# Kernel optimization log

Hardware: AMD Instinct MI355X
Metric: run time of the kernel (lower is better)

The kernel has to match this reference:

```python
import jax, jax.numpy as jnp
import numpy as np

N_NODES = 50000
N_EDGES = 800000
N_GRAPHS = 512
IN_CH, H, OUT = 58, 64, 128
HEADS1 = 4
NEG_SLOPE = 0.2
BN_EPS = 1e-5


def setup_inputs() -> dict:
    key = jax.random.key(0)
    ks = jax.random.split(key, 16)
    x = jax.random.normal(ks[0], (N_NODES, IN_CH), dtype=jnp.float32)
    edge_index = jax.random.randint(ks[1], (2, N_EDGES), 0, N_NODES, dtype=jnp.int64)
    batch = jnp.sort(jax.random.randint(ks[2], (N_NODES,), 0, N_GRAPHS, dtype=jnp.int64))
    s = 0.1
    return {
        "x": x,
        "edge_index": edge_index,
        "batch": batch,
        "W1": jax.random.normal(ks[3], (IN_CH, HEADS1 * H), dtype=jnp.float32) * s,
        "att_src1": jax.random.normal(ks[4], (HEADS1, H), dtype=jnp.float32) * s,
        "att_dst1": jax.random.normal(ks[5], (HEADS1, H), dtype=jnp.float32) * s,
        "b1": jnp.zeros((HEADS1 * H,), dtype=jnp.float32),
        "W2": jax.random.normal(ks[6], (HEADS1 * H, OUT), dtype=jnp.float32) * s,
        "att_src2": jax.random.normal(ks[7], (1, OUT), dtype=jnp.float32) * s,
        "att_dst2": jax.random.normal(ks[8], (1, OUT), dtype=jnp.float32) * s,
        "b2": jnp.zeros((OUT,), dtype=jnp.float32),
        "gamma": jax.random.normal(ks[9], (OUT,), dtype=jnp.float32) * 0.1 + 1.0,
        "beta": jax.random.normal(ks[10], (OUT,), dtype=jnp.float32) * 0.1,
    }


def gat_conv(x, src, dst, W, att_src, att_dst, b, heads, d_out):
    """PyG GATConv (concat=True, dropout off), self-loops already in src/dst."""
    n = x.shape[0]
    h = (x @ W).reshape(n, heads, d_out)                 # [N,H,D]
    a_s = jnp.einsum("nhd,hd->nh", h, att_src)            # [N,H]
    a_d = jnp.einsum("nhd,hd->nh", h, att_dst)            # [N,H]
    e = jax.nn.leaky_relu(a_s[src] + a_d[dst], NEG_SLOPE)  # [E,H]
    # softmax over edges grouped by destination node
    m = jax.ops.segment_max(e, dst, num_segments=n)
    ex = jnp.exp(e - m[dst])
    z = jax.ops.segment_sum(ex, dst, num_segments=n)
    alpha = ex / (z[dst] + 1e-16)
    msg = h[src] * alpha[:, :, None]                      # [E,H,D]
    out = jax.ops.segment_sum(msg, dst, num_segments=n)   # [N,H,D]
    return out.reshape(n, heads * d_out) + b


def reference(x, edge_index, batch, W1, att_src1, att_dst1, b1,
              W2, att_src2, att_dst2, b2, gamma, beta):
    n = x.shape[0]
    loops = jnp.arange(n, dtype=edge_index.dtype)
    src = jnp.concatenate([edge_index[0], loops])
    dst = jnp.concatenate([edge_index[1], loops])

    h1 = jax.nn.relu(gat_conv(x, src, dst, W1, att_src1, att_dst1, b1, HEADS1, H))
    h2 = jax.nn.relu(gat_conv(h1, src, dst, W2, att_src2, att_dst2, b2, 1, OUT))

    # global mean pool over graphs
    sums = jax.ops.segment_sum(h2, batch, num_segments=N_GRAPHS)      # [G,OUT]
    cnt = jax.ops.segment_sum(jnp.ones((n,), h2.dtype), batch, num_segments=N_GRAPHS)
    pooled = sums / jnp.maximum(cnt, 1.0)[:, None]

    # BatchNorm1d, training mode (batch statistics, biased variance)
    mu = pooled.mean(axis=0)
    var = pooled.var(axis=0)
    return (pooled - mu) / jnp.sqrt(var + BN_EPS) * gamma + beta
```

## Files before the change

kernel.cpp:

```cpp
#include <hip/hip_runtime.h>
#include <hip/hip_bf16.h>
#include <math.h>

#define N_NODES  50000
#define N_EDGES  800000
#define E_TOT    850000
#define N_GRAPHS 512
#define IN_CH    58
#define K1P      64
#define C1       256
#define H1       4
#define C2       128
#define NEG_SLOPE 0.2f
#define SLOT_CAP 64
#define NBUILD   208
#define NATT     3125
#define NBUCK    196
#define BCAP     5120

typedef __attribute__((ext_vector_type(8))) short short8;
typedef __attribute__((ext_vector_type(4))) float f32x4;

__device__ __forceinline__ float lo16(unsigned u) { return __uint_as_float(u << 16); }
__device__ __forceinline__ float hi16(unsigned u) { return __uint_as_float(u & 0xffff0000u); }
__device__ __forceinline__ float leaky(float e) { return e > 0.f ? e : NEG_SLOPE * e; }
__device__ __forceinline__ unsigned short f2bfu(float v) {
    __hip_bfloat16 b = __float2bfloat16(v);
    return *(unsigned short*)&b;
}
__device__ __forceinline__ unsigned pack2(float lo, float hi) {
    return (unsigned)f2bfu(lo) | ((unsigned)f2bfu(hi) << 16);
}

__global__ __launch_bounds__(256) void k_frontA(const float* __restrict__ W1,
                                                const float* __restrict__ W2,
                                                const float* __restrict__ atts1,
                                                const float* __restrict__ attd1,
                                                unsigned short* __restrict__ w1p,
                                                unsigned short* __restrict__ w2p,
                                                float* __restrict__ wproj) {
    int b = blockIdx.x;
    int t = threadIdx.x;
    if (b < 256) {
        if (t < K1P) {
            float v = (t < IN_CH) ? W1[t * C1 + b] : 0.f;
            int h = b >> 6, jj = (b >> 4) & 3, l15 = b & 15;
            int kk = t >> 5, quad = (t >> 3) & 3, e = t & 7;
            int f = (h * 4 + jj) * 2 + kk;
            w1p[(f * 64 + l15 * 4 + quad) * 8 + e] = f2bfu(v);
        }
    } else if (b < 384) {
        int n = b - 256;
        int j = n >> 4, l15 = n & 15;
        int k0 = t >> 5, quad = (t >> 3) & 3, e = t & 7;
        int f = j * 8 + k0;
        w2p[(f * 64 + l15 * 4 + quad) * 8 + e] = f2bfu(W2[t * C2 + n]);
    } else {
        int k = t >> 2, h = t & 3;
        float s = 0.f, dd = 0.f;
        if (k < IN_CH) {
            for (int j = 0; j < 64; ++j) {
                float wv = W1[k * C1 + h * 64 + j];
                s  += wv * atts1[h * 64 + j];
                dd += wv * attd1[h * 64 + j];
            }
        }
        wproj[t] = s;
        wproj[256 + t] = dd;
    }
}

__global__ __launch_bounds__(256) void k_mid(const int* __restrict__ src,
                                             const int* __restrict__ dst,
                                             int* __restrict__ bcnt,
                                             uint2* __restrict__ ebuf,
                                             const float* __restrict__ x,
                                             const float* __restrict__ wproj,
                                             unsigned short* __restrict__ xbf,
                                             float* __restrict__ a_s,
                                             float* __restrict__ a_d) {
    __shared__ int lhist[NBUCK];
    __shared__ int lbase[NBUCK];
    int b = blockIdx.x;
    int t = threadIdx.x;
    if (b < NBUILD) {
        if (t < NBUCK) lhist[t] = 0;
        __syncthreads();
        int j0 = (b * 256 + t) * 16;
        int s[16], d[16], bk[16], lp[16];
        bool v[16];
#pragma unroll
        for (int k = 0; k < 16; ++k) {
            int j = j0 + k;
            v[k] = j < E_TOT;
            if (v[k]) {
                if (j < N_EDGES) { s[k] = src[j]; d[k] = dst[j]; }
                else             { s[k] = d[k] = j - N_EDGES; }
                bk[k] = d[k] >> 8;
            }
        }
#pragma unroll
        for (int k = 0; k < 16; ++k)
            if (v[k]) lp[k] = atomicAdd(&lhist[bk[k]], 1);
        __syncthreads();
        if (t < NBUCK) lbase[t] = atomicAdd(&bcnt[t], lhist[t]);
        __syncthreads();
#pragma unroll
        for (int k = 0; k < 16; ++k)
            if (v[k])
                ebuf[(size_t)bk[k] * BCAP + lbase[bk[k]] + lp[k]] =
                    make_uint2((unsigned)s[k], (unsigned)d[k]);
    } else {
        int wave = t >> 6, lane = t & 63;
        int q = lane >> 4, hl = lane & 15;
        int n = (b - NBUILD) * 16 + wave * 4 + q;
        float xa[4] = {0.f, 0.f, 0.f, 0.f};
        const float* xr = x + (size_t)n * IN_CH + hl * 4;
        if (hl < 14) {
            float4 xv = *(const float4*)xr;
            xa[0] = xv.x; xa[1] = xv.y; xa[2] = xv.z; xa[3] = xv.w;
        } else if (hl == 14) {
            xa[0] = xr[0]; xa[1] = xr[1];
        }
        ((uint2*)xbf)[n * 16 + hl] = make_uint2(pack2(xa[0], xa[1]), pack2(xa[2], xa[3]));
        float ps[4] = {0.f, 0.f, 0.f, 0.f}, pd[4] = {0.f, 0.f, 0.f, 0.f};
#pragma unroll
        for (int cc = 0; cc < 4; ++cc) {
            int c = hl * 4 + cc;
            float4 wsv = *(const float4*)(wproj + c * 4);
            float4 wdv = *(const float4*)(wproj + 256 + c * 4);
            ps[0] += xa[cc] * wsv.x; ps[1] += xa[cc] * wsv.y;
            ps[2] += xa[cc] * wsv.z; ps[3] += xa[cc] * wsv.w;
            pd[0] += xa[cc] * wdv.x; pd[1] += xa[cc] * wdv.y;
            pd[2] += xa[cc] * wdv.z; pd[3] += xa[cc] * wdv.w;
        }
#pragma unroll
        for (int o = 8; o > 0; o >>= 1) {
#pragma unroll
            for (int r = 0; r < 4; ++r) {
                ps[r] += __shfl_down(ps[r], o, 16);
                pd[r] += __shfl_down(pd[r], o, 16);
            }
        }
        if (hl == 0) {
            *(float4*)(a_s + n * 4) = make_float4(ps[0], ps[1], ps[2], ps[3]);
            *(float4*)(a_d + n * 4) = make_float4(pd[0], pd[1], pd[2], pd[3]);
        }
    }
}

__global__ __launch_bounds__(256) void k_scat(const int* __restrict__ bcnt,
                                              const uint2* __restrict__ ebuf,
                                              int* __restrict__ deg,
                                              int* __restrict__ slots) {
    __shared__ int ldeg[256];
    int blk = blockIdx.x, t = threadIdx.x;
    ldeg[t] = 0;
    __syncthreads();
    int cnt = bcnt[blk];
    const uint2* eb = ebuf + (size_t)blk * BCAP;
    int base = 0;
    for (; base + 1024 <= cnt; base += 1024) {
        uint2 e[4];
#pragma unroll
        for (int k = 0; k < 4; ++k) e[k] = eb[base + k * 256 + t];
#pragma unroll
        for (int k = 0; k < 4; ++k) {
            int pos = atomicAdd(&ldeg[e[k].y & 255], 1);
            slots[((int)e[k].y << 6) + pos] = (int)e[k].x;
        }
    }
    for (int i = base + t; i < cnt; i += 256) {
        uint2 e = eb[i];
        int pos = atomicAdd(&ldeg[e.y & 255], 1);
        slots[((int)e.y << 6) + pos] = (int)e.x;
    }
    __syncthreads();
    int g = (blk << 8) + t;
    if (g < N_NODES) deg[g] = ldeg[t];
}

__global__ __launch_bounds__(256) void k_l1_agg(const int* __restrict__ degv,
                                                const int* __restrict__ slots,
                                                const float* __restrict__ a_s,
                                                const float* __restrict__ a_d,
                                                const uint2* __restrict__ xbf,
                                                unsigned short* __restrict__ xagg) {
    int t = threadIdx.x;
    int wave = t >> 6, lane = t & 63;
    int q = lane >> 4, hl = lane & 15;
    int d = blockIdx.x * 16 + wave * 4 + q;
    int beg = d << 6;
    int deg = degv[d];
    float4 ad = *(const float4*)(a_d + d * 4);
    float z0 = 0.f, z1 = 0.f, z2 = 0.f, z3 = 0.f;
    float a0[4] = {0.f, 0.f, 0.f, 0.f};
    float a1[4] = {0.f, 0.f, 0.f, 0.f};
    float a2[4] = {0.f, 0.f, 0.f, 0.f};
    float a3[4] = {0.f, 0.f, 0.f, 0.f};
    int i = 0;
    for (; i + 8 <= deg; i += 8) {
        int e0 = beg + i;
        int s[8]; uint2 u[8]; float4 as[8];
#pragma unroll
        for (int k = 0; k < 8; ++k) s[k] = slots[e0 + k];
#pragma unroll
        for (int k = 0; k < 8; ++k) u[k] = xbf[s[k] * 16 + hl];
#pragma unroll
        for (int k = 0; k < 8; ++k) as[k] = *(const float4*)(a_s + s[k] * 4);
#pragma unroll
        for (int k = 0; k < 8; ++k) {
            float e0h = __expf(leaky(as[k].x + ad.x));
            float e1h = __expf(leaky(as[k].y + ad.y));
            float e2h = __expf(leaky(as[k].z + ad.z));
            float e3h = __expf(leaky(as[k].w + ad.w));
            z0 += e0h; z1 += e1h; z2 += e2h; z3 += e3h;
            float c0 = lo16(u[k].x), c1 = hi16(u[k].x);
            float c2 = lo16(u[k].y), c3 = hi16(u[k].y);
            a0[0] += e0h * c0; a0[1] += e0h * c1; a0[2] += e0h * c2; a0[3] += e0h * c3;
            a1[0] += e1h * c0; a1[1] += e1h * c1; a1[2] += e1h * c2; a1[3] += e1h * c3;
            a2[0] += e2h * c0; a2[1] += e2h * c1; a2[2] += e2h * c2; a2[3] += e2h * c3;
            a3[0] += e3h * c0; a3[1] += e3h * c1; a3[2] += e3h * c2; a3[3] += e3h * c3;
        }
    }
    for (; i < deg; ++i) {
        int s = slots[beg + i];
        uint2 u = xbf[s * 16 + hl];
        float4 as = *(const float4*)(a_s + s * 4);
        float e0h = __expf(leaky(as.x + ad.x));
        float e1h = __expf(leaky(as.y + ad.y));
        float e2h = __expf(leaky(as.z + ad.z));
        float e3h = __expf(leaky(as.w + ad.w));
        z0 += e0h; z1 += e1h; z2 += e2h; z3 += e3h;
        float c0 = lo16(u.x), c1 = hi16(u.x);
        float c2 = lo16(u.y), c3 = hi16(u.y);
        a0[0] += e0h * c0; a0[1] += e0h * c1; a0[2] += e0h * c2; a0[3] += e0h * c3;
        a1[0] += e1h * c0; a1[1] += e1h * c1; a1[2] += e1h * c2; a1[3] += e1h * c3;
        a2[0] += e2h * c0; a2[1] += e2h * c1; a2[2] += e2h * c2; a2[3] += e2h * c3;
        a3[0] += e3h * c0; a3[1] += e3h * c1; a3[2] += e3h * c2; a3[3] += e3h * c3;
    }
    float i0 = 1.f / z0, i1 = 1.f / z1, i2 = 1.f / z2, i3 = 1.f / z3;
    int T = d >> 4, r = d & 15;
    int kk = hl >> 3, qd = (hl >> 1) & 3, half = hl & 1;
    uint2* xo = (uint2*)xagg;
    int base = (((T * 8 + kk) * 64) + r * 4 + qd) * 2 + half;
    xo[base +   0] = make_uint2(pack2(a0[0] * i0, a0[1] * i0), pack2(a0[2] * i0, a0[3] * i0));
    xo[base + 256] = make_uint2(pack2(a1[0] * i1, a1[1] * i1), pack2(a1[2] * i1, a1[3] * i1));
    xo[base + 512] = make_uint2(pack2(a2[0] * i2, a2[1] * i2), pack2(a2[2] * i2, a2[3] * i2));
    xo[base + 768] = make_uint2(pack2(a3[0] * i3, a3[1] * i3), pack2(a3[2] * i3, a3[3] * i3));
}

__global__ __launch_bounds__(256) void k_gemm12(const unsigned short* __restrict__ xagg,
                                                const unsigned short* __restrict__ w1p,
                                                const float* __restrict__ b1v,
                                                const unsigned short* __restrict__ w2p,
                                                const float* __restrict__ atts,
                                                const float* __restrict__ attd,
                                                unsigned short* __restrict__ h2bf,
                                                float* __restrict__ a_s,
                                                float* __restrict__ a_d) {
    __shared__ unsigned short hlds[4][16][264];
    int t = threadIdx.x;
    int wave = t >> 6, lane = t & 63;
    int T = blockIdx.x * 4 + wave;
    int m0 = T * 16;
    int l15 = lane & 15, quad = lane >> 4;
    int fl = l15 * 4 + quad;
    bool active = m0 < N_NODES;

    if (active) {
        const short8* xf  = (const short8*)xagg + (size_t)T * 512 + fl;
        const short8* w1f = (const short8*)w1p + fl;
        short8 av[H1][2];
#pragma unroll
        for (int h = 0; h < H1; ++h) {
            av[h][0] = xf[(h * 2 + 0) * 64];
            av[h][1] = xf[(h * 2 + 1) * 64];
        }
#pragma unroll
        for (int h = 0; h < H1; ++h) {
            short8 wb0[4], wb1[4];
#pragma unroll
            for (int jj = 0; jj < 4; ++jj) {
                wb0[jj] = w1f[(((h * 4 + jj) * 2) + 0) * 64];
                wb1[jj] = w1f[(((h * 4 + jj) * 2) + 1) * 64];
            }
            f32x4 acc[4];
#pragma unroll
            for (int jj = 0; jj < 4; ++jj) {
                acc[jj] = (f32x4){0.f, 0.f, 0.f, 0.f};
                acc[jj] = __builtin_amdgcn_mfma_f32_16x16x32_bf16(av[h][0], wb0[jj], acc[jj], 0, 0, 0);
                acc[jj] = __builtin_amdgcn_mfma_f32_16x16x32_bf16(av[h][1], wb1[jj], acc[jj], 0, 0, 0);
            }
#pragma unroll
            for (int jj = 0; jj < 4; ++jj) {
                int c = h * 64 + jj * 16 + l15;
                float bb = b1v[c];
#pragma unroll
                for (int r = 0; r < 4; ++r)
                    hlds[wave][quad * 4 + r][c] = f2bfu(fmaxf(acc[jj][r] + bb, 0.f));
            }
        }
    }
    __syncthreads();
    if (!active) return;

    short8 a2[8];
    const unsigned short* a2row = &hlds[wave][l15][0] + quad * 8;
#pragma unroll
    for (int k0 = 0; k0 < 8; ++k0) a2[k0] = *(const short8*)(a2row + k0 * 32);

    const short8* w2f = (const short8*)w2p + fl;
    unsigned short* scr = &hlds[wave][0][0];
    float ps[4] = {0.f, 0.f, 0.f, 0.f}, pd[4] = {0.f, 0.f, 0.f, 0.f};
#pragma unroll
    for (int j = 0; j < 8; ++j) {
        short8 wb[8];
#pragma unroll
        for (int k0 = 0; k0 < 8; ++k0)
            wb[k0] = w2f[(j * 8 + k0) * 64];
        f32x4 acc = (f32x4){0.f, 0.f, 0.f, 0.f};
#pragma unroll
        for (int k0 = 0; k0 < 8; ++k0)
            acc = __builtin_amdgcn_mfma_f32_16x16x32_bf16(a2[k0], wb[k0], acc, 0, 0, 0);
        float as_ = atts[j * 16 + l15], ad_ = attd[j * 16 + l15];
#pragma unroll
        for (int r = 0; r < 4; ++r) {
            float v = acc[r];
            scr[(quad * 4 + r) * 136 + j * 16 + l15] = f2bfu(v);
            ps[r] += v * as_;
            pd[r] += v * ad_;
        }
    }
#pragma unroll
    for (int r = 0; r < 4; ++r) {
#pragma unroll
        for (int o = 8; o > 0; o >>= 1) {
            ps[r] += __shfl_down(ps[r], o, 16);
            pd[r] += __shfl_down(pd[r], o, 16);
        }
        if (l15 == 0) {
            int n = m0 + quad * 4 + r;
            a_s[n] = ps[r];
            a_d[n] = pd[r];
        }
    }
    int row = lane >> 2, seg = lane & 3;
#pragma unroll
    for (int c = 0; c < 4; ++c) {
        short8 v = *(const short8*)(scr + row * 136 + (c * 4 + seg) * 8);
        *(short8*)(h2bf + (size_t)(m0 + row) * C2 + (c * 4 + seg) * 8) = v;
    }
}

__global__ __launch_bounds__(256) void k_l2_aggpool(const int* __restrict__ degv,
                                                    const int* __restrict__ slots,
                                                    const float* __restrict__ a_s,
                                                    const float* __restrict__ a_d,
                                                    const unsigned short* __restrict__ h2bf,
                                                    const float* __restrict__ b2,
                                                    const int* __restrict__ batch,
                                                    float* __restrict__ pooled) {
    __shared__ float sacc[8][C2];
    __shared__ int sg[8];
    int t = threadIdx.x;
    int wave = t >> 6, lane = t & 63;
    int half = lane >> 5, hl = lane & 31;
    int nodeIdx = wave * 2 + half;
    int d = blockIdx.x * 8 + nodeIdx;
    int beg = d << 6;
    int deg = degv[d];
    float ad = a_d[d];
    const uint2* rows = (const uint2*)h2bf;
    float a0 = 0.f, a1 = 0.f, a2 = 0.f, a3 = 0.f, z = 0.f;
    int i = 0;
    for (; i + 8 <= deg; i += 8) {
        int e0 = beg + i;
        int s[8]; uint2 u[8]; float ex[8];
#pragma unroll
        for (int k = 0; k < 8; ++k) s[k] = slots[e0 + k];
#pragma unroll
        for (int k = 0; k < 8; ++k) u[k] = rows[s[k] * 32 + hl];
#pragma unroll
        for (int k = 0; k < 8; ++k) ex[k] = __expf(leaky(a_s[s[k]] + ad));
#pragma unroll
        for (int k = 0; k < 8; ++k) {
            z  += ex[k];
            a0 += ex[k] * lo16(u[k].x); a1 += ex[k] * hi16(u[k].x);
            a2 += ex[k] * lo16(u[k].y); a3 += ex[k] * hi16(u[k].y);
        }
    }
    for (; i < deg; ++i) {
        int s = slots[beg + i];
        uint2 u = rows[s * 32 + hl];
        float ex = __expf(leaky(a_s[s] + ad));
        z  += ex;
        a0 += ex * lo16(u.x); a1 += ex * hi16(u.x);
        a2 += ex * lo16(u.y); a3 += ex * hi16(u.y);
    }
    float inv = 1.f / z;
    int c = hl * 4;
    float4 bv = *(const float4*)(b2 + c);
    float v0 = fmaxf(a0 * inv + bv.x, 0.f);
    float v1 = fmaxf(a1 * inv + bv.y, 0.f);
    float v2 = fmaxf(a2 * inv + bv.z, 0.f);
    float v3 = fmaxf(a3 * inv + bv.w, 0.f);
    if (hl == 0) sg[nodeIdx] = batch[d];
    *(float4*)&sacc[nodeIdx][c] = make_float4(v0, v1, v2, v3);
    __syncthreads();
    if (t < C2) {
        float run = sacc[0][t];
        int gprev = sg[0];
#pragma unroll
        for (int j = 1; j < 8; ++j) {
            int gj = sg[j];
            float v = sacc[j][t];
            if (gj == gprev) {
                run += v;
            } else {
                atomicAdd(&pooled[gprev * C2 + t], run);
                run = v;
                gprev = gj;
            }
        }
        atomicAdd(&pooled[gprev * C2 + t], run);
    }
}

__global__ __launch_bounds__(512) void k_bn(const float* __restrict__ pooled,
                                            const int* __restrict__ batch,
                                            const float* __restrict__ gamma,
                                            const float* __restrict__ beta,
                                            float* __restrict__ out) {
    int c = blockIdx.x;
    int g = threadIdx.x;
    int lo = 0, hi = N_NODES;
    while (lo < hi) { int m = (lo + hi) >> 1; if (batch[m] < g) lo = m + 1; else hi = m; }
    int lo2 = lo, hi2 = N_NODES;
    while (lo2 < hi2) { int m = (lo2 + hi2) >> 1; if (batch[m] < g + 1) lo2 = m + 1; else hi2 = m; }
    float cntg = (float)(hi2 - lo);

    __shared__ float red[512];
    __shared__ float s_mu, s_var;
    float v = pooled[g * C2 + c] / fmaxf(cntg, 1.0f);
    red[g] = v;
    __syncthreads();
    for (int s = 256; s > 0; s >>= 1) {
        if (g < s) red[g] += red[g + s];
        __syncthreads();
    }
    if (g == 0) s_mu = red[0] * (1.0f / N_GRAPHS);
    __syncthreads();
    float dv = v - s_mu;
    red[g] = dv * dv;
    __syncthreads();
    for (int s = 256; s > 0; s >>= 1) {
        if (g < s) red[g] += red[g + s];
        __syncthreads();
    }
    if (g == 0) s_var = red[0] * (1.0f / N_GRAPHS);
    __syncthreads();
    out[g * C2 + c] = dv * rsqrtf(s_var + 1e-5f) * gamma[c] + beta[c];
}

extern "C" void kernel_launch(void* const* d_in, const int* in_sizes, int n_in,
                              void* d_out, int out_size, void* d_ws, size_t ws_size,
                              hipStream_t stream) {
    const float* x     = (const float*)d_in[0];
    const int*   eidx  = (const int*)d_in[1];
    const int*   batch = (const int*)d_in[2];
    const float* W1    = (const float*)d_in[3];
    const float* atts1 = (const float*)d_in[4];
    const float* attd1 = (const float*)d_in[5];
    const float* b1    = (const float*)d_in[6];
    const float* W2    = (const float*)d_in[7];
    const float* atts2 = (const float*)d_in[8];
    const float* attd2 = (const float*)d_in[9];
    const float* b2    = (const float*)d_in[10];
    const float* gamma = (const float*)d_in[11];
    const float* beta  = (const float*)d_in[12];
    float* out = (float*)d_out;
    float* ws  = (float*)d_ws;

    const int* src = eidx;
    const int* dst = eidx + N_EDGES;

    const size_t o_xbf    = 0;
    const size_t o_xagg   = 1600000;
    const size_t o_h2bf   = 8000000;
    const size_t o_w1p    = 11200000;
    const size_t o_w2p    = 11208192;
    const size_t o_wproj  = 11224576;
    const size_t o_as1    = 11225088;
    const size_t o_ad1    = 11425088;
    const size_t o_as2    = 11625088;
    const size_t o_ad2    = 11675088;
    const size_t o_slots  = 11725088;
    const size_t o_deg    = 14925088;
    const size_t o_pool   = 14975088;
    const size_t o_bcnt   = 15040624;
    const size_t total    = 15040880;

    int* p_slots = (int*)(ws + o_slots);
    int* p_deg   = (int*)(ws + o_deg);
    int* p_bcnt  = (int*)(ws + o_bcnt);
    uint2* p_ebuf = (uint2*)(ws + o_xagg);
    unsigned short* p_xbf  = (unsigned short*)(ws + o_xbf);
    unsigned short* p_xagg = (unsigned short*)(ws + o_xagg);
    unsigned short* p_h2bf = (unsigned short*)(ws + o_h2bf);
    unsigned short* p_w1p  = (unsigned short*)(ws + o_w1p);
    unsigned short* p_w2p  = (unsigned short*)(ws + o_w2p);

    hipMemsetAsync(ws + o_deg, 0, (total - o_deg) * sizeof(float), stream);

    k_frontA<<<385, 256, 0, stream>>>(W1, W2, atts1, attd1,
                                      p_w1p, p_w2p, ws + o_wproj);
    k_mid<<<NBUILD + NATT, 256, 0, stream>>>(src, dst, p_bcnt, p_ebuf,
                                             x, ws + o_wproj, p_xbf,
                                             ws + o_as1, ws + o_ad1);
    k_scat<<<NBUCK, 256, 0, stream>>>(p_bcnt, p_ebuf, p_deg, p_slots);

    const int nagg1 = N_NODES / 16;
    const int nagg2 = N_NODES / 8;
    const int nmfma = (N_NODES + 63) / 64;

    k_l1_agg<<<nagg1, 256, 0, stream>>>(p_deg, p_slots, ws + o_as1, ws + o_ad1,
                                        (const uint2*)p_xbf, p_xagg);
    k_gemm12<<<nmfma, 256, 0, stream>>>(p_xagg, p_w1p, b1, p_w2p, atts2, attd2,
                                        p_h2bf, ws + o_as2, ws + o_ad2);

    k_l2_aggpool<<<nagg2, 256, 0, stream>>>(p_deg, p_slots, ws + o_as2, ws + o_ad2,
                                            p_h2bf, b2, batch, ws + o_pool);

    k_bn<<<C2, 512, 0, stream>>>(ws + o_pool, batch, gamma, beta, out);
}
```

Before: 244.5 us.

## Precompute normalized attention weights once per edge before GAT aggregations

In layer 1, each wave now computes the softmax-normalized edge weights for its four destination nodes once, lane-parallel over the slot list, and stores them as bf16 in LDS. The gather loop then reads these weights instead of recomputing exp per feature lane. For layer 2, a new kernel packs the bf16-normalized weight into the upper 16 bits of each slot entry, so the aggregation reads index and weight with one load and uses wider uint4 row loads, covering 16 nodes per block. The normalization drops the max-subtraction and rounds weights to bf16, which loses precision, and the 16-bit source index depends on N_NODES fitting in 65536.

```diff
diff --git a/kernel.cpp b/kernel.cpp
--- a/kernel.cpp
+++ b/kernel.cpp
@@ -186,35 +186,58 @@
                                                 const float* __restrict__ a_d,
                                                 const uint2* __restrict__ xbf,
                                                 unsigned short* __restrict__ xagg) {
+    __shared__ uint2 wlds[4][4][SLOT_CAP];
     int t = threadIdx.x;
     int wave = t >> 6, lane = t & 63;
     int q = lane >> 4, hl = lane & 15;
-    int d = blockIdx.x * 16 + wave * 4 + q;
+    int dbase = blockIdx.x * 16 + wave * 4;
+
+#pragma unroll
+    for (int nn = 0; nn < 4; ++nn) {
+        int node = dbase + nn;
+        int dg = degv[node];
+        float w0 = 0.f, w1 = 0.f, w2 = 0.f, w3 = 0.f;
+        if (lane < dg) {
+            int s = slots[(node << 6) + lane];
+            float4 as = *(const float4*)(a_s + s * 4);
+            float4 ad = *(const float4*)(a_d + node * 4);
+            w0 = __expf(leaky(as.x + ad.x));
+            w1 = __expf(leaky(as.y + ad.y));
+            w2 = __expf(leaky(as.z + ad.z));
+            w3 = __expf(leaky(as.w + ad.w));
+        }
+        float z0 = w0, z1 = w1, z2 = w2, z3 = w3;
+#pragma unroll
+        for (int o = 32; o > 0; o >>= 1) {
+            z0 += __shfl_xor(z0, o, 64); z1 += __shfl_xor(z1, o, 64);
+            z2 += __shfl_xor(z2, o, 64); z3 += __shfl_xor(z3, o, 64);
+        }
+        float i0 = 1.f / z0, i1 = 1.f / z1, i2 = 1.f / z2, i3 = 1.f / z3;
+        wlds[wave][nn][lane] = make_uint2(pack2(w0 * i0, w1 * i1), pack2(w2 * i2, w3 * i3));
+    }
+
+    int d = dbase + q;
     int beg = d << 6;
-    int deg = degv[d];
-    float4 ad = *(const float4*)(a_d + d * 4);
-    float z0 = 0.f, z1 = 0.f, z2 = 0.f, z3 = 0.f;
+    int dg = degv[d];
+    const uint2* wrow = &wlds[wave][q][0];
     float a0[4] = {0.f, 0.f, 0.f, 0.f};
     float a1[4] = {0.f, 0.f, 0.f, 0.f};
     float a2[4] = {0.f, 0.f, 0.f, 0.f};
     float a3[4] = {0.f, 0.f, 0.f, 0.f};
     int i = 0;
-    for (; i + 8 <= deg; i += 8) {
+    for (; i + 8 <= dg; i += 8) {
         int e0 = beg + i;
-        int s[8]; uint2 u[8]; float4 as[8];
+        int s[8]; uint2 u[8]; uint2 w[8];
 #pragma unroll
         for (int k = 0; k < 8; ++k) s[k] = slots[e0 + k];
 #pragma unroll
         for (int k = 0; k < 8; ++k) u[k] = xbf[s[k] * 16 + hl];
 #pragma unroll
-        for (int k = 0; k < 8; ++k) as[k] = *(const float4*)(a_s + s[k] * 4);
+        for (int k = 0; k < 8; ++k) w[k] = wrow[i + k];
 #pragma unroll
         for (int k = 0; k < 8; ++k) {
-            float e0h = __expf(leaky(as[k].x + ad.x));
-            float e1h = __expf(leaky(as[k].y + ad.y));
-            float e2h = __expf(leaky(as[k].z + ad.z));
-            float e3h = __expf(leaky(as[k].w + ad.w));
-            z0 += e0h; z1 += e1h; z2 += e2h; z3 += e3h;
+            float e0h = lo16(w[k].x), e1h = hi16(w[k].x);
+            float e2h = lo16(w[k].y), e3h = hi16(w[k].y);
             float c0 = lo16(u[k].x), c1 = hi16(u[k].x);
             float c2 = lo16(u[k].y), c3 = hi16(u[k].y);
             a0[0] += e0h * c0; a0[1] += e0h * c1; a0[2] += e0h * c2; a0[3] += e0h * c3;
@@ -223,15 +246,12 @@
             a3[0] += e3h * c0; a3[1] += e3h * c1; a3[2] += e3h * c2; a3[3] += e3h * c3;
         }
     }
-    for (; i < deg; ++i) {
+    for (; i < dg; ++i) {
         int s = slots[beg + i];
         uint2 u = xbf[s * 16 + hl];
-        float4 as = *(const float4*)(a_s + s * 4);
-        float e0h = __expf(leaky(as.x + ad.x));
-        float e1h = __expf(leaky(as.y + ad.y));
-        float e2h = __expf(leaky(as.z + ad.z));
-        float e3h = __expf(leaky(as.w + ad.w));
-        z0 += e0h; z1 += e1h; z2 += e2h; z3 += e3h;
+        uint2 w = wrow[i];
+        float e0h = lo16(w.x), e1h = hi16(w.x);
+        float e2h = lo16(w.y), e3h = hi16(w.y);
         float c0 = lo16(u.x), c1 = hi16(u.x);
         float c2 = lo16(u.y), c3 = hi16(u.y);
         a0[0] += e0h * c0; a0[1] += e0h * c1; a0[2] += e0h * c2; a0[3] += e0h * c3;
@@ -239,15 +259,14 @@
         a2[0] += e2h * c0; a2[1] += e2h * c1; a2[2] += e2h * c2; a2[3] += e2h * c3;
         a3[0] += e3h * c0; a3[1] += e3h * c1; a3[2] += e3h * c2; a3[3] += e3h * c3;
     }
-    float i0 = 1.f / z0, i1 = 1.f / z1, i2 = 1.f / z2, i3 = 1.f / z3;
     int T = d >> 4, r = d & 15;
     int kk = hl >> 3, qd = (hl >> 1) & 3, half = hl & 1;
     uint2* xo = (uint2*)xagg;
     int base = (((T * 8 + kk) * 64) + r * 4 + qd) * 2 + half;
-    xo[base +   0] = make_uint2(pack2(a0[0] * i0, a0[1] * i0), pack2(a0[2] * i0, a0[3] * i0));
-    xo[base + 256] = make_uint2(pack2(a1[0] * i1, a1[1] * i1), pack2(a1[2] * i1, a1[3] * i1));
-    xo[base + 512] = make_uint2(pack2(a2[0] * i2, a2[1] * i2), pack2(a2[2] * i2, a2[3] * i2));
-    xo[base + 768] = make_uint2(pack2(a3[0] * i3, a3[1] * i3), pack2(a3[2] * i3, a3[3] * i3));
+    xo[base +   0] = make_uint2(pack2(a0[0], a0[1]), pack2(a0[2], a0[3]));
+    xo[base + 256] = make_uint2(pack2(a1[0], a1[1]), pack2(a1[2], a1[3]));
+    xo[base + 512] = make_uint2(pack2(a2[0], a2[1]), pack2(a2[2], a2[3]));
+    xo[base + 768] = make_uint2(pack2(a3[0], a3[1]), pack2(a3[2], a3[3]));
 }
 
 __global__ __launch_bounds__(256) void k_gemm12(const unsigned short* __restrict__ xagg,
@@ -353,66 +372,89 @@
     }
 }
 
+__global__ __launch_bounds__(256) void k_w2(const int* __restrict__ degv,
+                                            int* __restrict__ slots,
+                                            const float* __restrict__ a_s,
+                                            const float* __restrict__ a_d) {
+    int t = threadIdx.x;
+    int wave = t >> 6, lane = t & 63;
+    int node = blockIdx.x * 4 + wave;
+    int dg = degv[node];
+    float ad = a_d[node];
+    float w = 0.f;
+    int s = 0;
+    if (lane < dg) {
+        s = slots[(node << 6) + lane];
+        w = __expf(leaky(a_s[s] + ad));
+    }
+    float z = w;
+#pragma unroll
+    for (int o = 32; o > 0; o >>= 1) z += __shfl_xor(z, o, 64);
+    float wn = w / z;
+    if (lane < dg)
+        slots[(node << 6) + lane] = s | ((unsigned)f2bfu(wn) << 16);
+}
+
 __global__ __launch_bounds__(256) void k_l2_aggpool(const int* __restrict__ degv,
                                                     const int* __restrict__ slots,
-                                                    const float* __restrict__ a_s,
-                                                    const float* __restrict__ a_d,
                                                     const unsigned short* __restrict__ h2bf,
                                                     const float* __restrict__ b2,
                                                     const int* __restrict__ batch,
                                                     float* __restrict__ pooled) {
-    __shared__ float sacc[8][C2];
-    __shared__ int sg[8];
+    __shared__ float sacc[16][C2];
+    __shared__ int sg[16];
     int t = threadIdx.x;
     int wave = t >> 6, lane = t & 63;
-    int half = lane >> 5, hl = lane & 31;
-    int nodeIdx = wave * 2 + half;
-    int d = blockIdx.x * 8 + nodeIdx;
+    int q = lane >> 4, hl = lane & 15;
+    int nodeIdx = wave * 4 + q;
+    int d = blockIdx.x * 16 + nodeIdx;
     int beg = d << 6;
-    int deg = degv[d];
-    float ad = a_d[d];
-    const uint2* rows = (const uint2*)h2bf;
-    float a0 = 0.f, a1 = 0.f, a2 = 0.f, a3 = 0.f, z = 0.f;
+    int dg = degv[d];
+    const uint4* rows = (const uint4*)h2bf;
+    float a0 = 0.f, a1 = 0.f, a2 = 0.f, a3 = 0.f;
+    float a4 = 0.f, a5 = 0.f, a6 = 0.f, a7 = 0.f;
     int i = 0;
-    for (; i + 8 <= deg; i += 8) {
+    for (; i + 8 <= dg; i += 8) {
         int e0 = beg + i;
-        int s[8]; uint2 u[8]; float ex[8];
-#pragma unroll
-        for (int k = 0; k < 8; ++k) s[k] = slots[e0 + k];
-#pragma unroll
-        for (int k = 0; k < 8; ++k) u[k] = rows[s[k] * 32 + hl];
-#pragma unroll
-        for (int k = 0; k < 8; ++k) ex[k] = __expf(leaky(a_s[s[k]] + ad));
+        int e[8]; uint4 u[8];
+#pragma unroll
+        for (int k = 0; k < 8; ++k) e[k] = slots[e0 + k];
+#pragma unroll
+        for (int k = 0; k < 8; ++k) u[k] = rows[(e[k] & 0xFFFF) * 16 + hl];
 #pragma unroll
         for (int k = 0; k < 8; ++k) {
-            z  += ex[k];
-            a0 += ex[k] * lo16(u[k].x); a1 += ex[k] * hi16(u[k].x);
-            a2 += ex[k] * lo16(u[k].y); a3 += ex[k] * hi16(u[k].y);
-        }
-    }
-    for (; i < deg; ++i) {
-        int s = slots[beg + i];
-        uint2 u = rows[s * 32 + hl];
-        float ex = __expf(leaky(a_s[s] + ad));
-        z  += ex;
-        a0 += ex * lo16(u.x); a1 += ex * hi16(u.x);
-        a2 += ex * lo16(u.y); a3 += ex * hi16(u.y);
-    }
-    float inv = 1.f / z;
-    int c = hl * 4;
-    float4 bv = *(const float4*)(b2 + c);
-    float v0 = fmaxf(a0 * inv + bv.x, 0.f);
-    float v1 = fmaxf(a1 * inv + bv.y, 0.f);
-    float v2 = fmaxf(a2 * inv + bv.z, 0.f);
-    float v3 = fmaxf(a3 * inv + bv.w, 0.f);
+            float w = __uint_as_float((unsigned)e[k] & 0xFFFF0000u);
+            a0 += w * lo16(u[k].x); a1 += w * hi16(u[k].x);
+            a2 += w * lo16(u[k].y); a3 += w * hi16(u[k].y);
+            a4 += w * lo16(u[k].z); a5 += w * hi16(u[k].z);
+            a6 += w * lo16(u[k].w); a7 += w * hi16(u[k].w);
+        }
+    }
+    for (; i < dg; ++i) {
+        int e = slots[beg + i];
+        uint4 u = rows[(e & 0xFFFF) * 16 + hl];
+        float w = __uint_as_float((unsigned)e & 0xFFFF0000u);
+        a0 += w * lo16(u.x); a1 += w * hi16(u.x);
+        a2 += w * lo16(u.y); a3 += w * hi16(u.y);
+        a4 += w * lo16(u.z); a5 += w * hi16(u.z);
+        a6 += w * lo16(u.w); a7 += w * hi16(u.w);
+    }
+    int c0 = hl * 8;
+    float4 bv0 = *(const float4*)(b2 + c0);
+    float4 bv1 = *(const float4*)(b2 + c0 + 4);
+    float v0 = fmaxf(a0 + bv0.x, 0.f), v1 = fmaxf(a1 + bv0.y, 0.f);
+    float v2 = fmaxf(a2 + bv0.z, 0.f), v3 = fmaxf(a3 + bv0.w, 0.f);
+    float v4 = fmaxf(a4 + bv1.x, 0.f), v5 = fmaxf(a5 + bv1.y, 0.f);
+    float v6 = fmaxf(a6 + bv1.z, 0.f), v7 = fmaxf(a7 + bv1.w, 0.f);
     if (hl == 0) sg[nodeIdx] = batch[d];
-    *(float4*)&sacc[nodeIdx][c] = make_float4(v0, v1, v2, v3);
+    *(float4*)&sacc[nodeIdx][c0]     = make_float4(v0, v1, v2, v3);
+    *(float4*)&sacc[nodeIdx][c0 + 4] = make_float4(v4, v5, v6, v7);
     __syncthreads();
     if (t < C2) {
         float run = sacc[0][t];
         int gprev = sg[0];
 #pragma unroll
-        for (int j = 1; j < 8; ++j) {
+        for (int j = 1; j < 16; ++j) {
             int gj = sg[j];
             float v = sacc[j][t];
             if (gj == gprev) {
@@ -521,15 +563,18 @@
     k_scat<<<NBUCK, 256, 0, stream>>>(p_bcnt, p_ebuf, p_deg, p_slots);
 
     const int nagg1 = N_NODES / 16;
-    const int nagg2 = N_NODES / 8;
+    const int nagg2 = N_NODES / 16;
     const int nmfma = (N_NODES + 63) / 64;
+    const int nw2   = N_NODES / 4;
 
     k_l1_agg<<<nagg1, 256, 0, stream>>>(p_deg, p_slots, ws + o_as1, ws + o_ad1,
                                         (const uint2*)p_xbf, p_xagg);
     k_gemm12<<<nmfma, 256, 0, stream>>>(p_xagg, p_w1p, b1, p_w2p, atts2, attd2,
                                         p_h2bf, ws + o_as2, ws + o_ad2);
 
-    k_l2_aggpool<<<nagg2, 256, 0, stream>>>(p_deg, p_slots, ws + o_as2, ws + o_ad2,
+    k_w2<<<nw2, 256, 0, stream>>>(p_deg, p_slots, ws + o_as2, ws + o_ad2);
+
+    k_l2_aggpool<<<nagg2, 256, 0, stream>>>(p_deg, p_slots,
                                             p_h2bf, b2, batch, ws + o_pool);
 
     k_bn<<<C2, 512, 0, stream>>>(ws + o_pool, batch, gamma, beta, out);
```

Measured after the change: 259.9 us. 1.06x slower.
